# Optimization experiments

Measured on AMD Instinct MI355X. Metric: run time of the kernel, lower is better.

The kernel has to match this reference:

```python
import jax, jax.numpy as jnp
import numpy as np

B, S, E, H = 2, 2048, 1024, 16
D = E // H

def setup_inputs() -> dict:
    key = jax.random.key(0)
    ks = jax.random.split(key, 5)
    return {
        "hidden_states": jax.random.normal(ks[0], (B, S, E), dtype=jnp.float32),
        "c_attn_w": jax.random.normal(ks[1], (E, 3 * E), dtype=jnp.float32) * 0.02,
        "c_attn_b": jax.random.normal(ks[2], (3 * E,), dtype=jnp.float32) * 0.02,
        "c_proj_w": jax.random.normal(ks[3], (E, E), dtype=jnp.float32) * 0.02,
        "c_proj_b": jax.random.normal(ks[4], (E,), dtype=jnp.float32) * 0.02,
    }

def reference(hidden_states, c_attn_w, c_attn_b, c_proj_w, c_proj_b):
    x = hidden_states                      # [B, S, E]
    b, s, _ = x.shape
    w_q, w_k, w_v = jnp.split(c_attn_w, 3, axis=1)   # each [E, E]
    q_b, k_b, v_b = jnp.split(c_attn_b, 3, axis=0)   # each [E]

    # value projection
    v = x @ w_v + v_b                                        # [B,S,E]
    v = v.reshape(b, s, H, D).transpose(0, 2, 1, 3)          # [B,H,S,D]

    # fused query: ((x Wq + qb) Wk^T + kb)
    q = (x @ w_q + q_b) @ w_k.T + k_b                        # [B,S,E]
    qh = q.reshape(b, s, H, D).transpose(0, 2, 1, 3)         # [B,H,S,D]

    # key side is RAW hidden states split per head
    kh = x.reshape(b, s, H, D).transpose(0, 2, 1, 3)         # [B,H,S,D]

    scale = 1.0 / jnp.float32(D) ** 0.5
    scores = jnp.einsum("bhqd,bhkd->bhqk",
                        qh.astype(jnp.float32),
                        kh.astype(jnp.float32)) * scale       # [B,H,S,S] fp32

    causal = jnp.tril(jnp.ones((s, s), dtype=bool))
    mask_value = jnp.finfo(jnp.float32).min
    scores = jnp.where(causal[None, None], scores, mask_value)

    probs = jax.nn.softmax(scores, axis=-1).astype(v.dtype)  # [B,H,S,S]

    out = jnp.einsum("bhqk,bhkd->bhqd", probs, v)            # [B,H,S,D]
    out = out.transpose(0, 2, 1, 3).reshape(b, s, E)         # [B,S,E]
    out = out @ c_proj_w + c_proj_b
    return out
```

## Files before the change

kernel.cpp:

```cpp
#include <hip/hip_runtime.h>

typedef __attribute__((ext_vector_type(8))) __bf16 bf16x8;
typedef __attribute__((ext_vector_type(4))) __bf16 bf16x4;
typedef __attribute__((ext_vector_type(4))) float f32x4;

typedef __attribute__((address_space(1))) void as1_void;
typedef __attribute__((address_space(3))) void as3_void;

__device__ __forceinline__ void gl_lds16(const void* g, void* l) {
    __builtin_amdgcn_global_load_lds((const as1_void*)g, (as3_void*)l, 16, 0, 0);
}

__device__ __forceinline__ const bf16x8* swz(const __bf16* base, int row, int chunk) {
    return (const bf16x8*)((const char*)base + row * 128 + ((chunk ^ (row & 7)) * 16));
}

#define QSCALE (0.125f * 1.44269504f)

__global__ __launch_bounds__(256) void prep_kernel(
    const float* __restrict__ x, const float* __restrict__ caw,
    const float* __restrict__ cab, const float* __restrict__ cpw,
    __bf16* __restrict__ xb, __bf16* __restrict__ wvt,
    __bf16* __restrict__ wkn, __bf16* __restrict__ wqn,
    __bf16* __restrict__ wpt, float* __restrict__ bqv)
{
    __shared__ float tile[32 * 33];
    int bid = blockIdx.x;
    int tid = threadIdx.x;
    if (bid < 1024) {
        int nt = bid >> 5, kt = bid & 31;
        int tx = tid & 31, ty = tid >> 5;
        int n0 = nt * 32, k0 = kt * 32;
#pragma unroll
        for (int i = 0; i < 4; ++i)
            tile[(ty + i * 8) * 33 + tx] = caw[(long)(k0 + ty + i * 8) * 3072 + 2048 + n0 + tx];
        __syncthreads();
#pragma unroll
        for (int i = 0; i < 4; ++i)
            wvt[(long)(n0 + ty + i * 8) * 1024 + k0 + tx] = (__bf16)tile[tx * 33 + ty + i * 8];
    } else if (bid < 2048) {
        int v = bid - 1024;
        int nt = v >> 5, kt = v & 31;
        int tx = tid & 31, ty = tid >> 5;
        int n0 = nt * 32, k0 = kt * 32;
#pragma unroll
        for (int i = 0; i < 4; ++i)
            tile[(ty + i * 8) * 33 + tx] = cpw[(long)(k0 + ty + i * 8) * 1024 + n0 + tx];
        __syncthreads();
#pragma unroll
        for (int i = 0; i < 4; ++i)
            wpt[(long)(n0 + ty + i * 8) * 1024 + k0 + tx] = (__bf16)tile[tx * 33 + ty + i * 8];
    } else if (bid < 3072) {
        int e = (bid - 2048) * 1024 + tid * 4;
        int n = e >> 10, k = e & 1023;
        float4 f = *(const float4*)(caw + (long)n * 3072 + 1024 + k);
        bf16x4 o = {(__bf16)f.x, (__bf16)f.y, (__bf16)f.z, (__bf16)f.w};
        *(bf16x4*)(wkn + e) = o;
    } else if (bid < 4096) {
        int e = (bid - 3072) * 1024 + tid * 4;
        int n = e >> 10, k = e & 1023;
        float4 f = *(const float4*)(caw + (long)n * 3072 + k);
        bf16x4 o = {(__bf16)f.x, (__bf16)f.y, (__bf16)f.z, (__bf16)f.w};
        *(bf16x4*)(wqn + e) = o;
    } else if (bid < 8192) {
        long e = (long)(bid - 4096) * 1024 + tid * 4;
        float4 f = *(const float4*)(x + e);
        bf16x4 o = {(__bf16)f.x, (__bf16)f.y, (__bf16)f.z, (__bf16)f.w};
        *(bf16x4*)(xb + e) = o;
    } else {
        int k = bid - 8192;
        int wave = tid >> 6, lane = tid & 63;
        float qv[16];
#pragma unroll
        for (int u = 0; u < 4; ++u) {
            float4 q4 = *(const float4*)(cab + u * 256 + lane * 4);
            qv[u * 4 + 0] = q4.x; qv[u * 4 + 1] = q4.y;
            qv[u * 4 + 2] = q4.z; qv[u * 4 + 3] = q4.w;
        }
        for (int i = 0; i < 16; ++i) {
            int n = k * 64 + wave * 16 + i;
            float s = 0.f;
#pragma unroll
            for (int u = 0; u < 4; ++u) {
                float4 w4 = *(const float4*)(caw + (long)n * 3072 + 1024 + u * 256 + lane * 4);
                s += w4.x * qv[u * 4 + 0] + w4.y * qv[u * 4 + 1]
                   + w4.z * qv[u * 4 + 2] + w4.w * qv[u * 4 + 3];
            }
#pragma unroll
            for (int off = 1; off < 64; off <<= 1) s += __shfl_xor(s, off);
            if (lane == 0) bqv[n] = (s + cab[1024 + n]) * QSCALE;
        }
        if (tid < 64) bqv[1024 + k * 64 + tid] = cab[2048 + k * 64 + tid];
    }
}

template <bool BF16OUT, int BN>
__global__ __launch_bounds__(256) void gemm_bt(
    const __bf16* __restrict__ A, int lda,
    const __bf16* __restrict__ B, int ldb,
    const float* __restrict__ bias,
    void* __restrict__ C, int ldc, int K, float oscale)
{
    constexpr int NT = BN / 32;
    __shared__ __bf16 As[128 * 64];
    __shared__ __bf16 Bs[BN * 64];
    const int tid = threadIdx.x;
    const int lane = tid & 63;
    const int wave = tid >> 6;
    const int quad = lane >> 4, l16 = lane & 15;
    const long m0 = (long)blockIdx.y * 128;
    const long n0 = (long)blockIdx.x * BN;
    const int wm = (wave >> 1) * 64, wn = (wave & 1) * (BN / 2);

    f32x4 acc[4][NT] = {};

    for (int k0 = 0; k0 < K; k0 += 64) {
#pragma unroll
        for (int c = tid; c < (128 + BN) * 8; c += 256) {
            int row = c >> 3, cc = (c & 7) ^ (row & 7);
            if (row < 128)
                gl_lds16(A + (m0 + row) * lda + k0 + cc * 8, As + c * 8);
            else
                gl_lds16(B + (n0 + row - 128) * ldb + k0 + cc * 8, Bs + (c - 1024) * 8);
        }
        __syncthreads();
#pragma unroll
        for (int kk = 0; kk < 2; ++kk) {
            bf16x8 af[4], bfr[NT];
#pragma unroll
            for (int i = 0; i < 4; ++i)
                af[i] = *swz(As, wm + i * 16 + l16, kk * 4 + quad);
#pragma unroll
            for (int j = 0; j < NT; ++j)
                bfr[j] = *swz(Bs, wn + j * 16 + l16, kk * 4 + quad);
#pragma unroll
            for (int i = 0; i < 4; ++i)
#pragma unroll
                for (int j = 0; j < NT; ++j)
                    acc[i][j] = __builtin_amdgcn_mfma_f32_16x16x32_bf16(af[i], bfr[j], acc[i][j], 0, 0, 0);
        }
        __syncthreads();
    }
#pragma unroll
    for (int i = 0; i < 4; ++i) {
        long row = m0 + wm + i * 16 + quad * 4;
#pragma unroll
        for (int j = 0; j < NT; ++j) {
            int col = (int)n0 + wn + j * 16 + l16;
            float bb = bias ? bias[col] : 0.f;
#pragma unroll
            for (int r = 0; r < 4; ++r) {
                float v = (acc[i][j][r] + bb) * oscale;
                if (BF16OUT)
                    ((__bf16*)C)[(row + r) * ldc + col] = (__bf16)v;
                else
                    ((float*)C)[(row + r) * ldc + col] = v;
            }
        }
    }
}

__global__ __launch_bounds__(256) void gemm_qv(
    const __bf16* __restrict__ A,
    const __bf16* __restrict__ B,
    const float* __restrict__ bias,
    __bf16* __restrict__ Qout,
    __bf16* __restrict__ VTout)
{
    __shared__ __bf16 smem[128 * 136];
    __bf16* As = smem;
    __bf16* Bs = smem + 8192;
    const int tid = threadIdx.x;
    const int lane = tid & 63;
    const int wave = tid >> 6;
    const int quad = lane >> 4, l16 = lane & 15;
    const long m0 = (long)blockIdx.y * 128;
    const long n0 = (long)blockIdx.x * 128;
    const int wm = (wave >> 1) * 64, wn = (wave & 1) * 64;

    f32x4 acc[4][4] = {};

    for (int k0 = 0; k0 < 1024; k0 += 64) {
#pragma unroll
        for (int c = tid; c < 2048; c += 256) {
            int row = c >> 3, cc = (c & 7) ^ (row & 7);
            if (row < 128)
                gl_lds16(A + (m0 + row) * 1024 + k0 + cc * 8, As + c * 8);
            else
                gl_lds16(B + (n0 + row - 128) * 1024 + k0 + cc * 8, Bs + (c - 1024) * 8);
        }
        __syncthreads();
#pragma unroll
        for (int kk = 0; kk < 2; ++kk) {
            bf16x8 af[4], bfr[4];
#pragma unroll
            for (int i = 0; i < 4; ++i)
                af[i] = *swz(As, wm + i * 16 + l16, kk * 4 + quad);
#pragma unroll
            for (int j = 0; j < 4; ++j)
                bfr[j] = *swz(Bs, wn + j * 16 + l16, kk * 4 + quad);
#pragma unroll
            for (int i = 0; i < 4; ++i)
#pragma unroll
                for (int j = 0; j < 4; ++j)
                    acc[i][j] = __builtin_amdgcn_mfma_f32_16x16x32_bf16(af[i], bfr[j], acc[i][j], 0, 0, 0);
        }
        __syncthreads();
    }

    if (n0 < 1024) {
#pragma unroll
        for (int i = 0; i < 4; ++i) {
            long row = m0 + wm + i * 16 + quad * 4;
#pragma unroll
            for (int j = 0; j < 4; ++j) {
                int col = (int)n0 + wn + j * 16 + l16;
                float bb = bias[col];
#pragma unroll
                for (int r = 0; r < 4; ++r)
                    Qout[(row + r) * 1024 + col] = (__bf16)(acc[i][j][r] + bb);
            }
        }
    } else {
        __syncthreads();
#pragma unroll
        for (int i = 0; i < 4; ++i) {
#pragma unroll
            for (int j = 0; j < 4; ++j) {
                int col = (int)n0 + wn + j * 16 + l16;
                float bb = bias[col];
                bf16x4 v;
#pragma unroll
                for (int r = 0; r < 4; ++r) v[r] = (__bf16)(acc[i][j][r] + bb);
                *(bf16x4*)(smem + (wn + j * 16 + l16) * 136 + wm + i * 16 + quad * 4) = v;
            }
        }
        __syncthreads();
        const int d0 = (int)n0 - 1024;
        const int bb = (int)(m0 >> 11);
        const int sl = (int)(m0 & 2047);
#pragma unroll
        for (int pass = 0; pass < 16; ++pass) {
            int idx = pass * 256 + tid;
            int n = idx >> 5;
            int mc = (idx & 31) * 4;
            bf16x4 v = *(const bf16x4*)(smem + n * 136 + mc);
            *(bf16x4*)(VTout + ((long)(bb * 1024 + d0 + n)) * 2048 + sl + mc) = v;
        }
    }
}

__global__ __launch_bounds__(256) void attn_kernel(
    const __bf16* __restrict__ Q,
    const __bf16* __restrict__ Xb,
    const __bf16* __restrict__ VT,
    __bf16* __restrict__ O)
{
    __shared__ __bf16 Ks[2 * 8192];
    __shared__ __bf16 Vs[2 * 8192];
    __shared__ __bf16 Ps[4 * 1024];
    const int tid = threadIdx.x;
    const int lane = tid & 63;
    const int wave = tid >> 6;
    const int quad = lane >> 4, l16 = lane & 15;
    const int qa = blockIdx.y;
    const int qb = 31 - qa;
    const int bh = blockIdx.x;
    const int b = bh >> 4, h = bh & 15;
    const long rowbase = (long)b * 2048;

    const int s0 = tid, s1 = tid + 256;
    const int c0 = ((s0 & 7) ^ ((s0 >> 3) & 7)) * 8;
    const int c1 = ((s1 & 7) ^ ((s1 >> 3) & 7)) * 8;

    bf16x8 ones;
#pragma unroll
    for (int i = 0; i < 8; ++i) ones[i] = (__bf16)1.0f;

    bf16x8 qfr[2][2];
#pragma unroll
    for (int t = 0; t < 2; ++t) {
        int qt = t ? qb : qa;
        const __bf16* qp = Q + (rowbase + qt * 64 + wave * 16 + l16) * 1024 + h * 64 + quad * 8;
        qfr[t][0] = *(const bf16x8*)(qp);
        qfr[t][1] = *(const bf16x8*)(qp + 32);
    }

    const __bf16* kp0 = Xb + (rowbase + (s0 >> 3)) * 1024 + h * 64 + c0;
    const __bf16* kp1 = Xb + (rowbase + (s1 >> 3)) * 1024 + h * 64 + c1;
    const __bf16* vp0 = VT + ((long)(b * 1024 + h * 64 + (s0 >> 3))) * 2048 + c0;
    const __bf16* vp1 = VT + ((long)(b * 1024 + h * 64 + (s1 >> 3))) * 2048 + c1;

    auto stage_tile = [&](int j, int buf, int sub) {
        __bf16* kd = Ks + buf * 8192 + sub * 4096;
        __bf16* vd = Vs + buf * 8192 + sub * 4096;
        gl_lds16(kp0 + (long)j * 65536, kd + s0 * 8);
        gl_lds16(kp1 + (long)j * 65536, kd + s1 * 8);
        gl_lds16(vp0 + j * 64, vd + s0 * 8);
        gl_lds16(vp1 + j * 64, vd + s1 * 8);
    };
    stage_tile(0, 0, 0);
    stage_tile(1, 0, 1);

    const int nouter = (qb + 2) >> 1;

    f32x4 oacc[2][4] = {};
    f32x4 lacc[2] = {};
    __bf16* Pw = Ps + wave * 1024;

    for (int jj = 0; jj < nouter; ++jj) {
        __syncthreads();
        if (jj + 1 < nouter) {
            stage_tile(2 * jj + 2, (jj + 1) & 1, 0);
            stage_tile(2 * jj + 3, (jj + 1) & 1, 1);
        }

#pragma unroll
        for (int sub = 0; sub < 2; ++sub) {
            const int j = 2 * jj + sub;
            if (j > qb) break;
            const __bf16* Kb = Ks + (jj & 1) * 8192 + sub * 4096;
            const __bf16* Vb = Vs + (jj & 1) * 8192 + sub * 4096;

            bf16x8 kf[2][4], vf[2][4];
#pragma unroll
            for (int kk = 0; kk < 2; ++kk)
#pragma unroll
                for (int kt = 0; kt < 4; ++kt) {
                    kf[kk][kt] = *swz(Kb, kt * 16 + l16, kk * 4 + quad);
                    vf[kk][kt] = *swz(Vb, kt * 16 + l16, kk * 4 + quad);
                }

#pragma unroll
            for (int t = 0; t < 2; ++t) {
                if (t == 0 && j > qa) continue;
                const int qt = t ? qb : qa;

                f32x4 sacc[4] = {};
#pragma unroll
                for (int kk = 0; kk < 2; ++kk)
#pragma unroll
                    for (int kt = 0; kt < 4; ++kt)
                        sacc[kt] = __builtin_amdgcn_mfma_f32_16x16x32_bf16(
                            kf[kk][kt], qfr[t][kk], sacc[kt], 0, 0, 0);

                if (j == qt) {
                    const int qloc = wave * 16 + l16;
#pragma unroll
                    for (int kt = 0; kt < 4; ++kt) {
                        bf16x4 pk;
#pragma unroll
                        for (int r = 0; r < 4; ++r) {
                            float s = sacc[kt][r];
                            if (kt * 16 + quad * 4 + r > qloc) s = -1e30f;
                            pk[r] = (__bf16)exp2f(s);
                        }
                        *(bf16x4*)((char*)Pw + l16 * 128 +
                                   (((kt * 2 + (quad >> 1)) ^ (l16 & 7)) * 16) + (quad & 1) * 8) = pk;
                    }
                } else {
#pragma unroll
                    for (int kt = 0; kt < 4; ++kt) {
                        bf16x4 pk;
#pragma unroll
                        for (int r = 0; r < 4; ++r)
                            pk[r] = (__bf16)exp2f(sacc[kt][r]);
                        *(bf16x4*)((char*)Pw + l16 * 128 +
                                   (((kt * 2 + (quad >> 1)) ^ (l16 & 7)) * 16) + (quad & 1) * 8) = pk;
                    }
                }

#pragma unroll
                for (int kk = 0; kk < 2; ++kk) {
                    bf16x8 pf = *swz(Pw, l16, kk * 4 + quad);
                    lacc[t] = __builtin_amdgcn_mfma_f32_16x16x32_bf16(ones, pf, lacc[t], 0, 0, 0);
#pragma unroll
                    for (int dt = 0; dt < 4; ++dt)
                        oacc[t][dt] = __builtin_amdgcn_mfma_f32_16x16x32_bf16(
                            vf[kk][dt], pf, oacc[t][dt], 0, 0, 0);
                }
            }
        }
    }

#pragma unroll
    for (int t = 0; t < 2; ++t) {
        const int qt = t ? qb : qa;
        float inv = 1.0f / lacc[t][0];
        long row = rowbase + qt * 64 + wave * 16 + l16;
#pragma unroll
        for (int dt = 0; dt < 4; ++dt) {
            bf16x4 ov;
#pragma unroll
            for (int r = 0; r < 4; ++r) ov[r] = (__bf16)(oacc[t][dt][r] * inv);
            *(bf16x4*)(O + row * 1024 + h * 64 + dt * 16 + quad * 4) = ov;
        }
    }
}

extern "C" void kernel_launch(void* const* d_in, const int* in_sizes, int n_in,
                              void* d_out, int out_size, void* d_ws, size_t ws_size,
                              hipStream_t stream) {
    const float* x   = (const float*)d_in[0];
    const float* caw = (const float*)d_in[1];
    const float* cab = (const float*)d_in[2];
    const float* cpw = (const float*)d_in[3];
    const float* cpb = (const float*)d_in[4];

    char* p = (char*)d_ws;
    auto alloc = [&](size_t bytes) {
        void* r = (void*)p;
        p += (bytes + 255) & ~(size_t)255;
        return r;
    };
    __bf16* xb    = (__bf16*)alloc(4096UL * 1024 * 2);
    __bf16* mtb   = (__bf16*)alloc(1024UL * 1024 * 2);
    __bf16* wvt   = (__bf16*)alloc(1024UL * 1024 * 2);
    __bf16* wkn   = (__bf16*)alloc(1024UL * 1024 * 2);
    __bf16* wqn   = (__bf16*)alloc(1024UL * 1024 * 2);
    __bf16* wpt   = (__bf16*)alloc(1024UL * 1024 * 2);
    float*  bqv   = (float*) alloc(2048UL * 4);
    __bf16* qbuf  = (__bf16*)alloc(4096UL * 1024 * 2);
    __bf16* vt    = (__bf16*)alloc(2048UL * 2048 * 2);
    __bf16* attn  = (__bf16*)alloc(4096UL * 1024 * 2);

    prep_kernel<<<8208, 256, 0, stream>>>(x, caw, cab, cpw, xb, wvt, wkn, wqn, wpt, bqv);

    gemm_bt<true, 32><<<dim3(32, 8), 256, 0, stream>>>(wkn, 1024, wqn, 1024, nullptr,
                                                       (void*)mtb, 1024, 1024, QSCALE);
    gemm_qv<<<dim3(16, 32), 256, 0, stream>>>(xb, mtb, bqv, qbuf, vt);
    attn_kernel<<<dim3(32, 16), 256, 0, stream>>>(qbuf, xb, vt, attn);
    gemm_bt<false, 64><<<dim3(16, 32), 256, 0, stream>>>(attn, 1024, wpt, 1024, cpb,
                                                         d_out, 1024, 1024, 1.0f);
    (void)in_sizes; (void)n_in; (void)out_size; (void)ws_size;
}
```

Before: 188.3 us.

## Fuse Wk·Wq product GEMM into prep kernel; split attention query tiles across wave groups

The separate bf16 casts of Wk and Wq and their standalone GEMM launch are removed. The prep kernel gains 64 blocks that read fp32 weights directly, convert them in shared memory and compute the Wk·Wq^T product with MFMA, which saves a launch and two intermediate buffers. Attention now runs 512 threads per block, with two groups of four waves each owning one of the paired query tiles instead of each wave handling both serially. This raises parallelism per block but leaves the two groups with unbalanced work, and the fused GEMM blocks use an unpipelined, padded-LDS loop.

```diff
diff --git a/kernel.cpp b/kernel.cpp
--- a/kernel.cpp
+++ b/kernel.cpp
@@ -21,13 +21,14 @@
     const float* __restrict__ x, const float* __restrict__ caw,
     const float* __restrict__ cab, const float* __restrict__ cpw,
     __bf16* __restrict__ xb, __bf16* __restrict__ wvt,
-    __bf16* __restrict__ wkn, __bf16* __restrict__ wqn,
-    __bf16* __restrict__ wpt, float* __restrict__ bqv)
+    __bf16* __restrict__ wpt, __bf16* __restrict__ mtb,
+    float* __restrict__ bqv)
 {
-    __shared__ float tile[32 * 33];
+    __shared__ __align__(16) char shm[20480];
     int bid = blockIdx.x;
     int tid = threadIdx.x;
     if (bid < 1024) {
+        float* tile = (float*)shm;
         int nt = bid >> 5, kt = bid & 31;
         int tx = tid & 31, ty = tid >> 5;
         int n0 = nt * 32, k0 = kt * 32;
@@ -39,6 +40,7 @@
         for (int i = 0; i < 4; ++i)
             wvt[(long)(n0 + ty + i * 8) * 1024 + k0 + tx] = (__bf16)tile[tx * 33 + ty + i * 8];
     } else if (bid < 2048) {
+        float* tile = (float*)shm;
         int v = bid - 1024;
         int nt = v >> 5, kt = v & 31;
         int tx = tid & 31, ty = tid >> 5;
@@ -50,25 +52,13 @@
 #pragma unroll
         for (int i = 0; i < 4; ++i)
             wpt[(long)(n0 + ty + i * 8) * 1024 + k0 + tx] = (__bf16)tile[tx * 33 + ty + i * 8];
-    } else if (bid < 3072) {
-        int e = (bid - 2048) * 1024 + tid * 4;
-        int n = e >> 10, k = e & 1023;
-        float4 f = *(const float4*)(caw + (long)n * 3072 + 1024 + k);
-        bf16x4 o = {(__bf16)f.x, (__bf16)f.y, (__bf16)f.z, (__bf16)f.w};
-        *(bf16x4*)(wkn + e) = o;
-    } else if (bid < 4096) {
-        int e = (bid - 3072) * 1024 + tid * 4;
-        int n = e >> 10, k = e & 1023;
-        float4 f = *(const float4*)(caw + (long)n * 3072 + k);
-        bf16x4 o = {(__bf16)f.x, (__bf16)f.y, (__bf16)f.z, (__bf16)f.w};
-        *(bf16x4*)(wqn + e) = o;
-    } else if (bid < 8192) {
-        long e = (long)(bid - 4096) * 1024 + tid * 4;
+    } else if (bid < 6144) {
+        long e = (long)(bid - 2048) * 1024 + tid * 4;
         float4 f = *(const float4*)(x + e);
         bf16x4 o = {(__bf16)f.x, (__bf16)f.y, (__bf16)f.z, (__bf16)f.w};
         *(bf16x4*)(xb + e) = o;
-    } else {
-        int k = bid - 8192;
+    } else if (bid < 6160) {
+        int k = bid - 6144;
         int wave = tid >> 6, lane = tid & 63;
         float qv[16];
 #pragma unroll
@@ -91,6 +81,52 @@
             if (lane == 0) bqv[n] = (s + cab[1024 + n]) * QSCALE;
         }
         if (tid < 64) bqv[1024 + k * 64 + tid] = cab[2048 + k * 64 + tid];
+    } else {
+        __bf16* Asm = (__bf16*)shm;
+        __bf16* Bsm = Asm + 5120;
+        int v = bid - 6160;
+        const long m0 = (long)(v >> 3) * 128;
+        const long n0 = (long)(v & 7) * 128;
+        const int lane = tid & 63, wave = tid >> 6;
+        const int quad = lane >> 4, l16 = lane & 15;
+        const int wm = (wave >> 1) * 64, wn = (wave & 1) * 64;
+        f32x4 acc[4][4] = {};
+        for (int k0 = 0; k0 < 1024; k0 += 32) {
+            for (int e = tid; e < 1024; e += 256) {
+                int row = e >> 3, c4 = e & 7;
+                float4 fa = *(const float4*)(caw + (m0 + row) * 3072 + 1024 + k0 + c4 * 4);
+                float4 fb = *(const float4*)(caw + (n0 + row) * 3072 + k0 + c4 * 4);
+                bf16x4 oa = {(__bf16)fa.x, (__bf16)fa.y, (__bf16)fa.z, (__bf16)fa.w};
+                bf16x4 ob = {(__bf16)fb.x, (__bf16)fb.y, (__bf16)fb.z, (__bf16)fb.w};
+                *(bf16x4*)(Asm + row * 40 + c4 * 4) = oa;
+                *(bf16x4*)(Bsm + row * 40 + c4 * 4) = ob;
+            }
+            __syncthreads();
+            bf16x8 af[4], bfr[4];
+#pragma unroll
+            for (int i = 0; i < 4; ++i)
+                af[i] = *(const bf16x8*)(Asm + (wm + i * 16 + l16) * 40 + quad * 8);
+#pragma unroll
+            for (int j = 0; j < 4; ++j)
+                bfr[j] = *(const bf16x8*)(Bsm + (wn + j * 16 + l16) * 40 + quad * 8);
+#pragma unroll
+            for (int i = 0; i < 4; ++i)
+#pragma unroll
+                for (int j = 0; j < 4; ++j)
+                    acc[i][j] = __builtin_amdgcn_mfma_f32_16x16x32_bf16(af[i], bfr[j], acc[i][j], 0, 0, 0);
+            __syncthreads();
+        }
+#pragma unroll
+        for (int i = 0; i < 4; ++i) {
+            long row = m0 + wm + i * 16 + quad * 4;
+#pragma unroll
+            for (int j = 0; j < 4; ++j) {
+                int col = (int)n0 + wn + j * 16 + l16;
+#pragma unroll
+                for (int r = 0; r < 4; ++r)
+                    mtb[(row + r) * 1024 + col] = (__bf16)(acc[i][j][r] * QSCALE);
+            }
+        }
     }
 }
 
@@ -250,7 +286,7 @@
     }
 }
 
-__global__ __launch_bounds__(256) void attn_kernel(
+__global__ __launch_bounds__(512) void attn_kernel(
     const __bf16* __restrict__ Q,
     const __bf16* __restrict__ Xb,
     const __bf16* __restrict__ VT,
@@ -258,54 +294,48 @@
 {
     __shared__ __bf16 Ks[2 * 8192];
     __shared__ __bf16 Vs[2 * 8192];
-    __shared__ __bf16 Ps[4 * 1024];
+    __shared__ __bf16 Ps[8 * 1024];
     const int tid = threadIdx.x;
     const int lane = tid & 63;
     const int wave = tid >> 6;
+    const int group = wave >> 2;
+    const int w4 = wave & 3;
     const int quad = lane >> 4, l16 = lane & 15;
     const int qa = blockIdx.y;
     const int qb = 31 - qa;
+    const int qt = group ? qb : qa;
     const int bh = blockIdx.x;
     const int b = bh >> 4, h = bh & 15;
     const long rowbase = (long)b * 2048;
 
-    const int s0 = tid, s1 = tid + 256;
+    const int s0 = tid;
     const int c0 = ((s0 & 7) ^ ((s0 >> 3) & 7)) * 8;
-    const int c1 = ((s1 & 7) ^ ((s1 >> 3) & 7)) * 8;
 
     bf16x8 ones;
 #pragma unroll
     for (int i = 0; i < 8; ++i) ones[i] = (__bf16)1.0f;
 
-    bf16x8 qfr[2][2];
-#pragma unroll
-    for (int t = 0; t < 2; ++t) {
-        int qt = t ? qb : qa;
-        const __bf16* qp = Q + (rowbase + qt * 64 + wave * 16 + l16) * 1024 + h * 64 + quad * 8;
-        qfr[t][0] = *(const bf16x8*)(qp);
-        qfr[t][1] = *(const bf16x8*)(qp + 32);
+    bf16x8 qfr[2];
+    {
+        const __bf16* qp = Q + (rowbase + qt * 64 + w4 * 16 + l16) * 1024 + h * 64 + quad * 8;
+        qfr[0] = *(const bf16x8*)(qp);
+        qfr[1] = *(const bf16x8*)(qp + 32);
     }
 
     const __bf16* kp0 = Xb + (rowbase + (s0 >> 3)) * 1024 + h * 64 + c0;
-    const __bf16* kp1 = Xb + (rowbase + (s1 >> 3)) * 1024 + h * 64 + c1;
     const __bf16* vp0 = VT + ((long)(b * 1024 + h * 64 + (s0 >> 3))) * 2048 + c0;
-    const __bf16* vp1 = VT + ((long)(b * 1024 + h * 64 + (s1 >> 3))) * 2048 + c1;
 
     auto stage_tile = [&](int j, int buf, int sub) {
-        __bf16* kd = Ks + buf * 8192 + sub * 4096;
-        __bf16* vd = Vs + buf * 8192 + sub * 4096;
-        gl_lds16(kp0 + (long)j * 65536, kd + s0 * 8);
-        gl_lds16(kp1 + (long)j * 65536, kd + s1 * 8);
-        gl_lds16(vp0 + j * 64, vd + s0 * 8);
-        gl_lds16(vp1 + j * 64, vd + s1 * 8);
+        gl_lds16(kp0 + (long)j * 65536, Ks + buf * 8192 + sub * 4096 + s0 * 8);
+        gl_lds16(vp0 + j * 64, Vs + buf * 8192 + sub * 4096 + s0 * 8);
     };
     stage_tile(0, 0, 0);
     stage_tile(1, 0, 1);
 
     const int nouter = (qb + 2) >> 1;
 
-    f32x4 oacc[2][4] = {};
-    f32x4 lacc[2] = {};
+    f32x4 oacc[4] = {};
+    f32x4 lacc = {};
     __bf16* Pw = Ps + wave * 1024;
 
     for (int jj = 0; jj < nouter; ++jj) {
@@ -318,7 +348,7 @@
 #pragma unroll
         for (int sub = 0; sub < 2; ++sub) {
             const int j = 2 * jj + sub;
-            if (j > qb) break;
+            if (j > qt) continue;
             const __bf16* Kb = Ks + (jj & 1) * 8192 + sub * 4096;
             const __bf16* Vb = Vs + (jj & 1) * 8192 + sub * 4096;
 
@@ -331,68 +361,60 @@
                     vf[kk][kt] = *swz(Vb, kt * 16 + l16, kk * 4 + quad);
                 }
 
-#pragma unroll
-            for (int t = 0; t < 2; ++t) {
-                if (t == 0 && j > qa) continue;
-                const int qt = t ? qb : qa;
-
-                f32x4 sacc[4] = {};
-#pragma unroll
-                for (int kk = 0; kk < 2; ++kk)
-#pragma unroll
-                    for (int kt = 0; kt < 4; ++kt)
-                        sacc[kt] = __builtin_amdgcn_mfma_f32_16x16x32_bf16(
-                            kf[kk][kt], qfr[t][kk], sacc[kt], 0, 0, 0);
-
-                if (j == qt) {
-                    const int qloc = wave * 16 + l16;
-#pragma unroll
-                    for (int kt = 0; kt < 4; ++kt) {
-                        bf16x4 pk;
-#pragma unroll
-                        for (int r = 0; r < 4; ++r) {
-                            float s = sacc[kt][r];
-                            if (kt * 16 + quad * 4 + r > qloc) s = -1e30f;
-                            pk[r] = (__bf16)exp2f(s);
-                        }
-                        *(bf16x4*)((char*)Pw + l16 * 128 +
-                                   (((kt * 2 + (quad >> 1)) ^ (l16 & 7)) * 16) + (quad & 1) * 8) = pk;
+            f32x4 sacc[4] = {};
+#pragma unroll
+            for (int kk = 0; kk < 2; ++kk)
+#pragma unroll
+                for (int kt = 0; kt < 4; ++kt)
+                    sacc[kt] = __builtin_amdgcn_mfma_f32_16x16x32_bf16(
+                        kf[kk][kt], qfr[kk], sacc[kt], 0, 0, 0);
+
+            if (j == qt) {
+                const int qloc = w4 * 16 + l16;
+#pragma unroll
+                for (int kt = 0; kt < 4; ++kt) {
+                    bf16x4 pk;
+#pragma unroll
+                    for (int r = 0; r < 4; ++r) {
+                        float s = sacc[kt][r];
+                        if (kt * 16 + quad * 4 + r > qloc) s = -1e30f;
+                        pk[r] = (__bf16)exp2f(s);
                     }
-                } else {
-#pragma unroll
-                    for (int kt = 0; kt < 4; ++kt) {
-                        bf16x4 pk;
-#pragma unroll
-                        for (int r = 0; r < 4; ++r)
-                            pk[r] = (__bf16)exp2f(sacc[kt][r]);
-                        *(bf16x4*)((char*)Pw + l16 * 128 +
-                                   (((kt * 2 + (quad >> 1)) ^ (l16 & 7)) * 16) + (quad & 1) * 8) = pk;
-                    }
+                    *(bf16x4*)((char*)Pw + l16 * 128 +
+                               (((kt * 2 + (quad >> 1)) ^ (l16 & 7)) * 16) + (quad & 1) * 8) = pk;
                 }
-
-#pragma unroll
-                for (int kk = 0; kk < 2; ++kk) {
-                    bf16x8 pf = *swz(Pw, l16, kk * 4 + quad);
-                    lacc[t] = __builtin_amdgcn_mfma_f32_16x16x32_bf16(ones, pf, lacc[t], 0, 0, 0);
-#pragma unroll
-                    for (int dt = 0; dt < 4; ++dt)
-                        oacc[t][dt] = __builtin_amdgcn_mfma_f32_16x16x32_bf16(
-                            vf[kk][dt], pf, oacc[t][dt], 0, 0, 0);
+            } else {
+#pragma unroll
+                for (int kt = 0; kt < 4; ++kt) {
+                    bf16x4 pk;
+#pragma unroll
+                    for (int r = 0; r < 4; ++r)
+                        pk[r] = (__bf16)exp2f(sacc[kt][r]);
+                    *(bf16x4*)((char*)Pw + l16 * 128 +
+                               (((kt * 2 + (quad >> 1)) ^ (l16 & 7)) * 16) + (quad & 1) * 8) = pk;
                 }
             }
-        }
-    }
-
-#pragma unroll
-    for (int t = 0; t < 2; ++t) {
-        const int qt = t ? qb : qa;
-        float inv = 1.0f / lacc[t][0];
-        long row = rowbase + qt * 64 + wave * 16 + l16;
+
+#pragma unroll
+            for (int kk = 0; kk < 2; ++kk) {
+                bf16x8 pf = *swz(Pw, l16, kk * 4 + quad);
+                lacc = __builtin_amdgcn_mfma_f32_16x16x32_bf16(ones, pf, lacc, 0, 0, 0);
+#pragma unroll
+                for (int dt = 0; dt < 4; ++dt)
+                    oacc[dt] = __builtin_amdgcn_mfma_f32_16x16x32_bf16(
+                        vf[kk][dt], pf, oacc[dt], 0, 0, 0);
+            }
+        }
+    }
+
+    {
+        float inv = 1.0f / lacc[0];
+        long row = rowbase + qt * 64 + w4 * 16 + l16;
 #pragma unroll
         for (int dt = 0; dt < 4; ++dt) {
             bf16x4 ov;
 #pragma unroll
-            for (int r = 0; r < 4; ++r) ov[r] = (__bf16)(oacc[t][dt][r] * inv);
+            for (int r = 0; r < 4; ++r) ov[r] = (__bf16)(oacc[dt][r] * inv);
             *(bf16x4*)(O + row * 1024 + h * 64 + dt * 16 + quad * 4) = ov;
         }
     }
@@ -416,20 +438,15 @@
     __bf16* xb    = (__bf16*)alloc(4096UL * 1024 * 2);
     __bf16* mtb   = (__bf16*)alloc(1024UL * 1024 * 2);
     __bf16* wvt   = (__bf16*)alloc(1024UL * 1024 * 2);
-    __bf16* wkn   = (__bf16*)alloc(1024UL * 1024 * 2);
-    __bf16* wqn   = (__bf16*)alloc(1024UL * 1024 * 2);
     __bf16* wpt   = (__bf16*)alloc(1024UL * 1024 * 2);
     float*  bqv   = (float*) alloc(2048UL * 4);
     __bf16* qbuf  = (__bf16*)alloc(4096UL * 1024 * 2);
     __bf16* vt    = (__bf16*)alloc(2048UL * 2048 * 2);
     __bf16* attn  = (__bf16*)alloc(4096UL * 1024 * 2);
 
-    prep_kernel<<<8208, 256, 0, stream>>>(x, caw, cab, cpw, xb, wvt, wkn, wqn, wpt, bqv);
-
-    gemm_bt<true, 32><<<dim3(32, 8), 256, 0, stream>>>(wkn, 1024, wqn, 1024, nullptr,
-                                                       (void*)mtb, 1024, 1024, QSCALE);
+    prep_kernel<<<6224, 256, 0, stream>>>(x, caw, cab, cpw, xb, wvt, wpt, mtb, bqv);
     gemm_qv<<<dim3(16, 32), 256, 0, stream>>>(xb, mtb, bqv, qbuf, vt);
-    attn_kernel<<<dim3(32, 16), 256, 0, stream>>>(qbuf, xb, vt, attn);
+    attn_kernel<<<dim3(32, 16), 512, 0, stream>>>(qbuf, xb, vt, attn);
     gemm_bt<false, 64><<<dim3(16, 32), 256, 0, stream>>>(attn, 1024, wpt, 1024, cpb,
                                                          d_out, 1024, 1024, 1.0f);
     (void)in_sizes; (void)n_in; (void)out_size; (void)ws_size;
```

New measurement: 214.0 us. 1.14x slower.

## Split paired query tiles across two wave groups in 512-thread attention blocks

Applied to the files above, without the earlier changes.

The attention kernel now launches 512 threads per block. Each group of four waves handles one of the two paired causal query tiles (qa or qb), where previously each wave processed both tiles in sequence. K/V staging is spread over twice as many threads, and per-wave accumulator state is halved. This is meant to double wave-level parallelism and lower register pressure, but the qa group sits idle once its tile is done while still joining the barriers, and the larger LDS P buffer adds shared-memory use.

```diff
diff --git a/kernel.cpp b/kernel.cpp
--- a/kernel.cpp
+++ b/kernel.cpp
@@ -250,7 +250,7 @@
     }
 }
 
-__global__ __launch_bounds__(256) void attn_kernel(
+__global__ __launch_bounds__(512) void attn_kernel(
     const __bf16* __restrict__ Q,
     const __bf16* __restrict__ Xb,
     const __bf16* __restrict__ VT,
@@ -258,54 +258,48 @@
 {
     __shared__ __bf16 Ks[2 * 8192];
     __shared__ __bf16 Vs[2 * 8192];
-    __shared__ __bf16 Ps[4 * 1024];
+    __shared__ __bf16 Ps[8 * 1024];
     const int tid = threadIdx.x;
     const int lane = tid & 63;
     const int wave = tid >> 6;
+    const int group = wave >> 2;
+    const int w4 = wave & 3;
     const int quad = lane >> 4, l16 = lane & 15;
     const int qa = blockIdx.y;
     const int qb = 31 - qa;
+    const int qt = group ? qb : qa;
     const int bh = blockIdx.x;
     const int b = bh >> 4, h = bh & 15;
     const long rowbase = (long)b * 2048;
 
-    const int s0 = tid, s1 = tid + 256;
+    const int s0 = tid;
     const int c0 = ((s0 & 7) ^ ((s0 >> 3) & 7)) * 8;
-    const int c1 = ((s1 & 7) ^ ((s1 >> 3) & 7)) * 8;
 
     bf16x8 ones;
 #pragma unroll
     for (int i = 0; i < 8; ++i) ones[i] = (__bf16)1.0f;
 
-    bf16x8 qfr[2][2];
-#pragma unroll
-    for (int t = 0; t < 2; ++t) {
-        int qt = t ? qb : qa;
-        const __bf16* qp = Q + (rowbase + qt * 64 + wave * 16 + l16) * 1024 + h * 64 + quad * 8;
-        qfr[t][0] = *(const bf16x8*)(qp);
-        qfr[t][1] = *(const bf16x8*)(qp + 32);
+    bf16x8 qfr[2];
+    {
+        const __bf16* qp = Q + (rowbase + qt * 64 + w4 * 16 + l16) * 1024 + h * 64 + quad * 8;
+        qfr[0] = *(const bf16x8*)(qp);
+        qfr[1] = *(const bf16x8*)(qp + 32);
     }
 
     const __bf16* kp0 = Xb + (rowbase + (s0 >> 3)) * 1024 + h * 64 + c0;
-    const __bf16* kp1 = Xb + (rowbase + (s1 >> 3)) * 1024 + h * 64 + c1;
     const __bf16* vp0 = VT + ((long)(b * 1024 + h * 64 + (s0 >> 3))) * 2048 + c0;
-    const __bf16* vp1 = VT + ((long)(b * 1024 + h * 64 + (s1 >> 3))) * 2048 + c1;
 
     auto stage_tile = [&](int j, int buf, int sub) {
-        __bf16* kd = Ks + buf * 8192 + sub * 4096;
-        __bf16* vd = Vs + buf * 8192 + sub * 4096;
-        gl_lds16(kp0 + (long)j * 65536, kd + s0 * 8);
-        gl_lds16(kp1 + (long)j * 65536, kd + s1 * 8);
-        gl_lds16(vp0 + j * 64, vd + s0 * 8);
-        gl_lds16(vp1 + j * 64, vd + s1 * 8);
+        gl_lds16(kp0 + (long)j * 65536, Ks + buf * 8192 + sub * 4096 + s0 * 8);
+        gl_lds16(vp0 + j * 64, Vs + buf * 8192 + sub * 4096 + s0 * 8);
     };
     stage_tile(0, 0, 0);
     stage_tile(1, 0, 1);
 
     const int nouter = (qb + 2) >> 1;
 
-    f32x4 oacc[2][4] = {};
-    f32x4 lacc[2] = {};
+    f32x4 oacc[4] = {};
+    f32x4 lacc = {};
     __bf16* Pw = Ps + wave * 1024;
 
     for (int jj = 0; jj < nouter; ++jj) {
@@ -318,7 +312,7 @@
 #pragma unroll
         for (int sub = 0; sub < 2; ++sub) {
             const int j = 2 * jj + sub;
-            if (j > qb) break;
+            if (j > qt) continue;
             const __bf16* Kb = Ks + (jj & 1) * 8192 + sub * 4096;
             const __bf16* Vb = Vs + (jj & 1) * 8192 + sub * 4096;
 
@@ -331,68 +325,60 @@
                     vf[kk][kt] = *swz(Vb, kt * 16 + l16, kk * 4 + quad);
                 }
 
-#pragma unroll
-            for (int t = 0; t < 2; ++t) {
-                if (t == 0 && j > qa) continue;
-                const int qt = t ? qb : qa;
-
-                f32x4 sacc[4] = {};
-#pragma unroll
-                for (int kk = 0; kk < 2; ++kk)
-#pragma unroll
-                    for (int kt = 0; kt < 4; ++kt)
-                        sacc[kt] = __builtin_amdgcn_mfma_f32_16x16x32_bf16(
-                            kf[kk][kt], qfr[t][kk], sacc[kt], 0, 0, 0);
-
-                if (j == qt) {
-                    const int qloc = wave * 16 + l16;
-#pragma unroll
-                    for (int kt = 0; kt < 4; ++kt) {
-                        bf16x4 pk;
-#pragma unroll
-                        for (int r = 0; r < 4; ++r) {
-                            float s = sacc[kt][r];
-                            if (kt * 16 + quad * 4 + r > qloc) s = -1e30f;
-                            pk[r] = (__bf16)exp2f(s);
-                        }
-                        *(bf16x4*)((char*)Pw + l16 * 128 +
-                                   (((kt * 2 + (quad >> 1)) ^ (l16 & 7)) * 16) + (quad & 1) * 8) = pk;
+            f32x4 sacc[4] = {};
+#pragma unroll
+            for (int kk = 0; kk < 2; ++kk)
+#pragma unroll
+                for (int kt = 0; kt < 4; ++kt)
+                    sacc[kt] = __builtin_amdgcn_mfma_f32_16x16x32_bf16(
+                        kf[kk][kt], qfr[kk], sacc[kt], 0, 0, 0);
+
+            if (j == qt) {
+                const int qloc = w4 * 16 + l16;
+#pragma unroll
+                for (int kt = 0; kt < 4; ++kt) {
+                    bf16x4 pk;
+#pragma unroll
+                    for (int r = 0; r < 4; ++r) {
+                        float s = sacc[kt][r];
+                        if (kt * 16 + quad * 4 + r > qloc) s = -1e30f;
+                        pk[r] = (__bf16)exp2f(s);
                     }
-                } else {
-#pragma unroll
-                    for (int kt = 0; kt < 4; ++kt) {
-                        bf16x4 pk;
-#pragma unroll
-                        for (int r = 0; r < 4; ++r)
-                            pk[r] = (__bf16)exp2f(sacc[kt][r]);
-                        *(bf16x4*)((char*)Pw + l16 * 128 +
-                                   (((kt * 2 + (quad >> 1)) ^ (l16 & 7)) * 16) + (quad & 1) * 8) = pk;
-                    }
+                    *(bf16x4*)((char*)Pw + l16 * 128 +
+                               (((kt * 2 + (quad >> 1)) ^ (l16 & 7)) * 16) + (quad & 1) * 8) = pk;
                 }
-
-#pragma unroll
-                for (int kk = 0; kk < 2; ++kk) {
-                    bf16x8 pf = *swz(Pw, l16, kk * 4 + quad);
-                    lacc[t] = __builtin_amdgcn_mfma_f32_16x16x32_bf16(ones, pf, lacc[t], 0, 0, 0);
-#pragma unroll
-                    for (int dt = 0; dt < 4; ++dt)
-                        oacc[t][dt] = __builtin_amdgcn_mfma_f32_16x16x32_bf16(
-                            vf[kk][dt], pf, oacc[t][dt], 0, 0, 0);
+            } else {
+#pragma unroll
+                for (int kt = 0; kt < 4; ++kt) {
+                    bf16x4 pk;
+#pragma unroll
+                    for (int r = 0; r < 4; ++r)
+                        pk[r] = (__bf16)exp2f(sacc[kt][r]);
+                    *(bf16x4*)((char*)Pw + l16 * 128 +
+                               (((kt * 2 + (quad >> 1)) ^ (l16 & 7)) * 16) + (quad & 1) * 8) = pk;
                 }
             }
-        }
-    }
-
-#pragma unroll
-    for (int t = 0; t < 2; ++t) {
-        const int qt = t ? qb : qa;
-        float inv = 1.0f / lacc[t][0];
-        long row = rowbase + qt * 64 + wave * 16 + l16;
+
+#pragma unroll
+            for (int kk = 0; kk < 2; ++kk) {
+                bf16x8 pf = *swz(Pw, l16, kk * 4 + quad);
+                lacc = __builtin_amdgcn_mfma_f32_16x16x32_bf16(ones, pf, lacc, 0, 0, 0);
+#pragma unroll
+                for (int dt = 0; dt < 4; ++dt)
+                    oacc[dt] = __builtin_amdgcn_mfma_f32_16x16x32_bf16(
+                        vf[kk][dt], pf, oacc[dt], 0, 0, 0);
+            }
+        }
+    }
+
+    {
+        float inv = 1.0f / lacc[0];
+        long row = rowbase + qt * 64 + w4 * 16 + l16;
 #pragma unroll
         for (int dt = 0; dt < 4; ++dt) {
             bf16x4 ov;
 #pragma unroll
-            for (int r = 0; r < 4; ++r) ov[r] = (__bf16)(oacc[t][dt][r] * inv);
+            for (int r = 0; r < 4; ++r) ov[r] = (__bf16)(oacc[dt][r] * inv);
             *(bf16x4*)(O + row * 1024 + h * 64 + dt * 16 + quad * 4) = ov;
         }
     }
@@ -429,7 +415,7 @@
     gemm_bt<true, 32><<<dim3(32, 8), 256, 0, stream>>>(wkn, 1024, wqn, 1024, nullptr,
                                                        (void*)mtb, 1024, 1024, QSCALE);
     gemm_qv<<<dim3(16, 32), 256, 0, stream>>>(xb, mtb, bqv, qbuf, vt);
-    attn_kernel<<<dim3(32, 16), 256, 0, stream>>>(qbuf, xb, vt, attn);
+    attn_kernel<<<dim3(32, 16), 512, 0, stream>>>(qbuf, xb, vt, attn);
     gemm_bt<false, 64><<<dim3(16, 32), 256, 0, stream>>>(attn, 1024, wpt, 1024, cpb,
                                                          d_out, 1024, 1024, 1.0f);
     (void)in_sizes; (void)n_in; (void)out_size; (void)ws_size;
```

Result: faster. 181.4 us (-3.6%).
